# Kernel tuning notes

Hardware: AMD Instinct MI355X
Metric: run time of the kernel (lower is better)

The kernel has to match this reference:

```python
import jax, jax.numpy as jnp
import numpy as np
import math

NUM_HEADS = 8
KEY_SIZE = 512
EMBED_DIM = 256
BN_EPS = 1e-5


def batchnorm2d_train(x, w, b):
    # x: [B, H, N, hd]; channel axis = 1 (heads). Training-mode batch stats
    # over (B, N, hd), biased variance, as in torch BatchNorm2d forward.
    mean = jnp.mean(x, axis=(0, 2, 3), keepdims=True)
    var = jnp.mean((x - mean) ** 2, axis=(0, 2, 3), keepdims=True)
    xn = (x - mean) * jax.lax.rsqrt(var + BN_EPS)
    return xn * w[None, :, None, None] + b[None, :, None, None]


def l2_normalize(x, axis, eps=1e-12):
    # matches F.normalize(p=2): x / max(||x||, eps)
    n = jnp.sqrt(jnp.sum(x * x, axis=axis, keepdims=True))
    return x / jnp.maximum(n, eps)


def sparsemax(z, axis):
    # Euclidean projection onto the simplex along `axis` (Martins & Astudillo).
    K = z.shape[axis]
    z = z - jnp.max(z, axis=axis, keepdims=True)  # shift-invariant, for stability
    zs = jnp.flip(jnp.sort(z, axis=axis), axis=axis)  # descending sort
    rng_shape = [1] * z.ndim
    rng_shape[axis] = K
    rng = jnp.arange(1, K + 1, dtype=z.dtype).reshape(rng_shape)
    css = jnp.cumsum(zs, axis=axis)
    support = (1.0 + rng * zs) > css
    k_z = jnp.sum(support.astype(jnp.int32), axis=axis, keepdims=True)  # support size >= 1
    tau_sum = jnp.take_along_axis(css, k_z - 1, axis=axis)
    tau = (tau_sum - 1.0) / k_z.astype(z.dtype)
    return jnp.maximum(z - tau, 0.0)


def setup_inputs() -> dict:
    key = jax.random.key(0)
    k1, k2, k3 = jax.random.split(key, 3)
    B, N, C = 8, 1024, EMBED_DIM
    lim = 1.0 / math.sqrt(C)  # torch Linear default init range
    x = jax.random.normal(k1, (B, N, C), dtype=jnp.float32)
    qw = jax.random.uniform(k2, (KEY_SIZE, C), jnp.float32, -lim, lim)
    kw = jax.random.uniform(k3, (KEY_SIZE, C), jnp.float32, -lim, lim)
    bn_weight = jnp.ones((NUM_HEADS,), jnp.float32)
    bn_bias = jnp.zeros((NUM_HEADS,), jnp.float32)
    return {"x": x, "qw": qw, "kw": kw, "bn_weight": bn_weight, "bn_bias": bn_bias}


def reference(x, qw, kw, bn_weight, bn_bias):
    B, N, C = x.shape
    H = NUM_HEADS
    hd = KEY_SIZE // H
    q = jnp.einsum('bnc,kc->bnk', x, qw)  # [B,N,key_size]
    k = jnp.einsum('bnc,kc->bnk', x, kw)
    Q = q.reshape(B, N, H, hd).transpose(0, 2, 1, 3)  # [B,H,N,hd]
    K = k.reshape(B, N, H, hd).transpose(0, 2, 1, 3)
    Q = batchnorm2d_train(Q, bn_weight, bn_bias)
    K = batchnorm2d_train(K, bn_weight, bn_bias)
    Q = l2_normalize(Q, axis=3)
    K = l2_normalize(K, axis=3)
    scores = jnp.einsum('bhnd,bhmd->bhnm', Q, K) / math.sqrt(C)  # scale by sqrt(embeded_dim)
    scores = scores.transpose(0, 2, 1, 3).reshape(B, N, H * N)  # [B,N,H*N]
    # dropout is identity in eval mode
    return sparsemax(scores, axis=1)
```

## Files before the change

kernel.cpp:

```cpp
#include <hip/hip_runtime.h>
#include <math.h>

#define S_STAT 0
#define S_Q    32
#define S_K    (32 + 4194304)
#define S_PL   (32 + 8388608)
#define PLSZ   4194304

typedef unsigned short ushort;
typedef unsigned int uint;
typedef __attribute__((ext_vector_type(8))) short short8;
typedef __attribute__((ext_vector_type(16))) float floatx16;
typedef __attribute__((ext_vector_type(2))) float f32x2;

__device__ __forceinline__ float wave_sum(float v) {
#pragma unroll
    for (int m = 1; m < 64; m <<= 1) v += __shfl_xor(v, m);
    return v;
}

__device__ __forceinline__ ushort f2bf(float f) {
    uint u = __float_as_uint(f);
    uint r = (u + 0x7fffu + ((u >> 16) & 1u)) >> 16;
    return (ushort)r;
}

__global__ __launch_bounds__(64) void k0_zero(float* __restrict__ ws) {
    if (threadIdx.x < 32) ws[S_STAT + threadIdx.x] = 0.0f;
}

__global__ __launch_bounds__(256) void k_pre(const float* __restrict__ x,
                                             const float* __restrict__ qw,
                                             const float* __restrict__ kw,
                                             float* __restrict__ ws) {
    ushort* base = (ushort*)(ws + S_PL) + 4 * PLSZ;
    ushort* XH = base;
    ushort* XL = XH + 2097152;
    ushort* WH = XL + 2097152;
    ushort* WL = WH + 262144;
    const int bid = blockIdx.x;
    const int tid = threadIdx.x;
    const float* __restrict__ src;
    ushort *dh, *dl;
    int idx4;
    if (bid < 2048)      { src = x;  dh = XH;           dl = XL;           idx4 = bid * 256 + tid; }
    else if (bid < 2176) { src = qw; dh = WH;           dl = WL;           idx4 = (bid - 2048) * 256 + tid; }
    else                 { src = kw; dh = WH + 131072;  dl = WL + 131072;  idx4 = (bid - 2176) * 256 + tid; }
    const float4 v = *(const float4*)(src + (size_t)idx4 * 4);
    ushort4 hv, lv;
    {
        hv.x = f2bf(v.x); lv.x = f2bf(v.x - __uint_as_float(((uint)hv.x) << 16));
        hv.y = f2bf(v.y); lv.y = f2bf(v.y - __uint_as_float(((uint)hv.y) << 16));
        hv.z = f2bf(v.z); lv.z = f2bf(v.z - __uint_as_float(((uint)hv.z) << 16));
        hv.w = f2bf(v.w); lv.w = f2bf(v.w - __uint_as_float(((uint)hv.w) << 16));
    }
    *(ushort4*)(dh + (size_t)idx4 * 4) = hv;
    *(ushort4*)(dl + (size_t)idx4 * 4) = lv;
}

__global__ __launch_bounds__(256, 2) void k1_mfma(float* __restrict__ ws) {
    const ushort* base = (const ushort*)(ws + S_PL) + 4 * PLSZ;
    const ushort* __restrict__ XH = base;
    const ushort* __restrict__ XL = XH + 2097152;
    const ushort* __restrict__ WH = XL + 2097152;
    const ushort* __restrict__ WL = WH + 262144;
    const int t = threadIdx.x;
    const int l = t & 63;
    const int w = t >> 6;
    const int rw = w & 1, cw = w >> 1;
    const int row0 = blockIdx.x * 128 + rw * 64;
    const int col0 = blockIdx.y * 128 + cw * 64;
    const int lane31 = l & 31;
    const int kb8 = (l >> 5) * 8;

    floatx16 acc[2][2] = {};
#pragma unroll 4
    for (int kc = 0; kc < 256; kc += 16) {
        short8 ah[2], al[2], bh[2], bl[2];
#pragma unroll
        for (int rt = 0; rt < 2; ++rt) {
            const size_t o = (size_t)(row0 + rt * 32 + lane31) * 256 + kc + kb8;
            ah[rt] = *(const short8*)(XH + o);
            al[rt] = *(const short8*)(XL + o);
        }
#pragma unroll
        for (int ct = 0; ct < 2; ++ct) {
            const size_t o = (size_t)(col0 + ct * 32 + lane31) * 256 + kc + kb8;
            bh[ct] = *(const short8*)(WH + o);
            bl[ct] = *(const short8*)(WL + o);
        }
#pragma unroll
        for (int rt = 0; rt < 2; ++rt)
#pragma unroll
            for (int ct = 0; ct < 2; ++ct) {
                acc[rt][ct] = __builtin_amdgcn_mfma_f32_32x32x16_bf16(ah[rt], bh[ct], acc[rt][ct], 0, 0, 0);
                acc[rt][ct] = __builtin_amdgcn_mfma_f32_32x32x16_bf16(al[rt], bh[ct], acc[rt][ct], 0, 0, 0);
                acc[rt][ct] = __builtin_amdgcn_mfma_f32_32x32x16_bf16(ah[rt], bl[ct], acc[rt][ct], 0, 0, 0);
            }
    }

    const bool is_q = (col0 < 512);
    float* __restrict__ outp = ws + (is_q ? S_Q : S_K);
    const int cbase = col0 & 511;
    const int rsub = 4 * (l >> 5);
    float s1 = 0.f, s2 = 0.f;
#pragma unroll
    for (int rt = 0; rt < 2; ++rt)
#pragma unroll
        for (int ct = 0; ct < 2; ++ct)
#pragma unroll
            for (int e = 0; e < 16; ++e) {
                const int r = row0 + rt * 32 + rsub + (e & 3) + 8 * (e >> 2);
                const int c = cbase + ct * 32 + lane31;
                const float v = acc[rt][ct][e];
                outp[(size_t)r * 512 + c] = v;
                s1 += v; s2 += v * v;
            }
    s1 = wave_sum(s1);
    s2 = wave_sum(s2);
    if (l == 0) {
        const int head = (cbase >> 6) & 7;
        const int sb = (is_q ? 0 : 16) + head;
        atomicAdd(ws + S_STAT + sb, s1);
        atomicAdd(ws + S_STAT + sb + 8, s2);
    }
}

__global__ __launch_bounds__(256) void k3_norm(const float* __restrict__ bnw,
                                               const float* __restrict__ bnb,
                                               float* __restrict__ ws) {
    const int t = threadIdx.x;
    const int w = t >> 6, l = t & 63;
    const int nb = blockIdx.x;
    const int bh = blockIdx.y;
    const int b = bh >> 3, h = bh & 7;
    const int z = blockIdx.z;
    const float* __restrict__ in = ws + (z ? S_K : S_Q);
    const float* st = ws + S_STAT + (z ? 16 : 0);
    ushort* __restrict__ PH = (ushort*)(ws + S_PL) + (z ? 2 * PLSZ : 0) + (size_t)bh * 65536;
    ushort* __restrict__ PL = PH + PLSZ;
    const float inv_m = 1.0f / 524288.0f;
    const float mean  = st[h] * inv_m;
    const float var   = st[8 + h] * inv_m - mean * mean;
    const float alpha = rsqrtf(var + 1e-5f) * bnw[h];
    const float beta  = bnb[h] - mean * alpha;
    const float scale = z ? 0.0625f : 1.0f;

#pragma unroll 1
    for (int i = 0; i < 16; ++i) {
        const int n = nb * 64 + w * 16 + i;
        float v = in[(size_t)(b * 1024 + n) * 512 + h * 64 + l];
        v = fmaf(v, alpha, beta);
        float ss = wave_sum(v * v);
        v = v / fmaxf(sqrtf(ss), 1e-12f) * scale;
        ushort h16 = f2bf(v);
        float hif = __uint_as_float(((uint)h16) << 16);
        ushort l16 = f2bf(v - hif);
        const int idx = n * 64 + l;
        PH[idx] = h16;
        PL[idx] = l16;
    }
}

__global__ __launch_bounds__(256, 3) void k4_attn(const float* __restrict__ ws,
                                                  float* __restrict__ out) {
    __shared__ float part[4][4][32];
    const int t = threadIdx.x;
    const int l = t & 63;
    const int w = t >> 6;
    const int bid = blockIdx.x;
    const int bh = bid >> 5;
    const int j  = bid & 31;
    const int m0 = ((j & 7) << 7) + ((j >> 3) << 5);
    const int b = bh >> 3, h = bh & 7;
    const ushort* __restrict__ QH = (const ushort*)(ws + S_PL);
    const ushort* __restrict__ QL = QH + PLSZ;
    const ushort* __restrict__ KH = QH + 2 * PLSZ;
    const ushort* __restrict__ KL = QH + 3 * PLSZ;

    const int row = l & 31;
    const int kb8 = l >> 5;

    floatx16 acc[8] = {};

    const size_t koff = (size_t)(bh * 1024 + m0 + row) * 64 + kb8 * 8;
#pragma unroll
    for (int r = 0; r < 8; ++r) {
        const size_t qoff = (size_t)(bh * 1024 + w * 256 + r * 32 + row) * 64 + kb8 * 8;
#pragma unroll
        for (int ks = 0; ks < 4; ++ks) {
            short8 ah = *(const short8*)(QH + qoff + ks * 16);
            short8 al = *(const short8*)(QL + qoff + ks * 16);
            short8 kh = *(const short8*)(KH + koff + ks * 16);
            short8 kl = *(const short8*)(KL + koff + ks * 16);
            acc[r] = __builtin_amdgcn_mfma_f32_32x32x16_bf16(ah, kh, acc[r], 0, 0, 0);
            acc[r] = __builtin_amdgcn_mfma_f32_32x32x16_bf16(al, kh, acc[r], 0, 0, 0);
            acc[r] = __builtin_amdgcn_mfma_f32_32x32x16_bf16(ah, kl, acc[r], 0, 0, 0);
        }
    }

    const int col = row;

    {
        f32x2 sv = {0.f, 0.f};
#pragma unroll
        for (int r = 0; r < 8; ++r)
#pragma unroll
            for (int p = 0; p < 8; ++p) {
                f32x2 z2 = { acc[r][2 * p], acc[r][2 * p + 1] };
                sv += z2;
            }
        float vsuml = sv.x + sv.y;
        vsuml += __shfl_xor(vsuml, 32);
        if (l < 32) part[2][w][col] = vsuml;
    }
    __syncthreads();
    const float vsum = part[2][0][col] + part[2][1][col]
                     + part[2][2][col] + part[2][3][col];

    float tcur = (vsum - 1.0f) * (1.0f / 1024.0f);
    float tprev = tcur, sprev = 0.f;
#pragma unroll 1
    for (int it = 0; it < 6; ++it) {
        f32x2 s2v = {0.f, 0.f};
#pragma unroll
        for (int r = 0; r < 8; ++r) {
            f32x2 sr = {0.f, 0.f};
#pragma unroll
            for (int p = 0; p < 8; ++p) {
                f32x2 z2 = { acc[r][2 * p], acc[r][2 * p + 1] };
                f32x2 d = z2 - tcur;
                d.x = fmaxf(d.x, 0.f);
                d.y = fmaxf(d.y, 0.f);
                sr += d;
            }
            s2v += sr;
        }
        float sl = s2v.x + s2v.y;
        sl += __shfl_xor(sl, 32);
        if (l < 32) part[it & 1][w][col] = sl;
        __syncthreads();
        const float s = part[it & 1][0][col] + part[it & 1][1][col]
                      + part[it & 1][2][col] + part[it & 1][3][col];
        const float g = s - 1.0f;
        float step;
        if (it == 0) {
            step = g * (1.0f / 1024.0f);
        } else {
            const float denom = sprev - s;
            step = (denom > 1e-30f) ? g * (tcur - tprev) / denom : 0.f;
        }
        step = fmaxf(step, 0.f);
        tprev = tcur; sprev = s;
        tcur += step;
    }

    float cntl = 0.f, ssml = 0.f;
#pragma unroll
    for (int r = 0; r < 8; ++r)
#pragma unroll
        for (int e = 0; e < 16; ++e) {
            const float zz = acc[r][e];
            if (zz > tcur) { cntl += 1.f; ssml += zz; }
        }
    cntl += __shfl_xor(cntl, 32);
    ssml += __shfl_xor(ssml, 32);
    if (l < 32) { part[2][w][col] = cntl; part[3][w][col] = ssml; }
    __syncthreads();
    const float cnt  = part[2][0][col] + part[2][1][col] + part[2][2][col] + part[2][3][col];
    const float ssum = part[3][0][col] + part[3][1][col] + part[3][2][col] + part[3][3][col];
    const float tau = (ssum - 1.0f) / cnt;

    float* __restrict__ ob = out + (size_t)b * 1024 * 8192 + h * 1024 + m0 + col;
    const int nbase = w * 256 + 4 * kb8;
#pragma unroll
    for (int r = 0; r < 8; ++r)
#pragma unroll
        for (int e = 0; e < 16; ++e) {
            const int n = nbase + r * 32 + (e & 3) + 8 * (e >> 2);
            ob[(size_t)n * 8192] = fmaxf(acc[r][e] - tau, 0.f);
        }
}

extern "C" void kernel_launch(void* const* d_in, const int* in_sizes, int n_in,
                              void* d_out, int out_size, void* d_ws, size_t ws_size,
                              hipStream_t stream) {
    (void)in_sizes; (void)n_in; (void)out_size; (void)ws_size;
    const float* x   = (const float*)d_in[0];
    const float* qw  = (const float*)d_in[1];
    const float* kw  = (const float*)d_in[2];
    const float* bnw = (const float*)d_in[3];
    const float* bnb = (const float*)d_in[4];
    float* ws  = (float*)d_ws;
    float* out = (float*)d_out;

    hipLaunchKernelGGL(k0_zero, dim3(1), dim3(64), 0, stream, ws);
    hipLaunchKernelGGL(k_pre, dim3(2304), dim3(256), 0, stream, x, qw, kw, ws);
    hipLaunchKernelGGL(k1_mfma, dim3(64, 8), dim3(256), 0, stream, ws);
    hipLaunchKernelGGL(k3_norm, dim3(16, 64, 2), dim3(256), 0, stream, bnw, bnb, ws);
    hipLaunchKernelGGL(k4_attn, dim3(2048), dim3(256), 0, stream, ws, out);
}
```

Measured before the change: 442.8 us.

## Fold stats zeroing into k_pre, vectorize norm kernel, trim sparsemax iterations

Zeroing of the BN statistics buffer moves into the first block of k_pre, which removes a separate kernel launch. The norm kernel now has each thread load four floats and reduce over 16 lanes, so loads and stores are wider and the full-wave shuffle reductions are shorter. The iterative threshold search in the sparsemax stage runs five iterations instead of six. That cuts compute, but the threshold may converge less precisely and change outputs.

Result: no change. 440.1 us, median of 2 (-0.6%).

```diff
diff --git a/kernel.cpp b/kernel.cpp
--- a/kernel.cpp
+++ b/kernel.cpp
@@ -12,6 +12,7 @@
 typedef __attribute__((ext_vector_type(8))) short short8;
 typedef __attribute__((ext_vector_type(16))) float floatx16;
 typedef __attribute__((ext_vector_type(2))) float f32x2;
+typedef __attribute__((ext_vector_type(4))) float f32x4;
 
 __device__ __forceinline__ float wave_sum(float v) {
 #pragma unroll
@@ -23,10 +24,6 @@
     uint u = __float_as_uint(f);
     uint r = (u + 0x7fffu + ((u >> 16) & 1u)) >> 16;
     return (ushort)r;
-}
-
-__global__ __launch_bounds__(64) void k0_zero(float* __restrict__ ws) {
-    if (threadIdx.x < 32) ws[S_STAT + threadIdx.x] = 0.0f;
 }
 
 __global__ __launch_bounds__(256) void k_pre(const float* __restrict__ x,
@@ -40,6 +37,7 @@
     ushort* WL = WH + 262144;
     const int bid = blockIdx.x;
     const int tid = threadIdx.x;
+    if (bid == 0 && tid < 32) ws[S_STAT + tid] = 0.0f;
     const float* __restrict__ src;
     ushort *dh, *dl;
     int idx4;
@@ -131,6 +129,7 @@
                                                float* __restrict__ ws) {
     const int t = threadIdx.x;
     const int w = t >> 6, l = t & 63;
+    const int g = l >> 4, l16 = l & 15;
     const int nb = blockIdx.x;
     const int bh = blockIdx.y;
     const int b = bh >> 3, h = bh & 7;
@@ -146,19 +145,30 @@
     const float beta  = bnb[h] - mean * alpha;
     const float scale = z ? 0.0625f : 1.0f;
 
+    const int d0 = l16 * 4;
 #pragma unroll 1
-    for (int i = 0; i < 16; ++i) {
-        const int n = nb * 64 + w * 16 + i;
-        float v = in[(size_t)(b * 1024 + n) * 512 + h * 64 + l];
-        v = fmaf(v, alpha, beta);
-        float ss = wave_sum(v * v);
-        v = v / fmaxf(sqrtf(ss), 1e-12f) * scale;
-        ushort h16 = f2bf(v);
-        float hif = __uint_as_float(((uint)h16) << 16);
-        ushort l16 = f2bf(v - hif);
-        const int idx = n * 64 + l;
-        PH[idx] = h16;
-        PL[idx] = l16;
+    for (int i = 0; i < 4; ++i) {
+        const int n = nb * 64 + w * 16 + i * 4 + g;
+        const f32x4 vv = *(const f32x4*)&in[(size_t)(b * 1024 + n) * 512 + h * 64 + d0];
+        float v0 = fmaf(vv.x, alpha, beta);
+        float v1 = fmaf(vv.y, alpha, beta);
+        float v2 = fmaf(vv.z, alpha, beta);
+        float v3 = fmaf(vv.w, alpha, beta);
+        float ss = v0 * v0 + v1 * v1 + v2 * v2 + v3 * v3;
+        ss += __shfl_xor(ss, 1);
+        ss += __shfl_xor(ss, 2);
+        ss += __shfl_xor(ss, 4);
+        ss += __shfl_xor(ss, 8);
+        const float inv = scale / fmaxf(sqrtf(ss), 1e-12f);
+        v0 *= inv; v1 *= inv; v2 *= inv; v3 *= inv;
+        ushort4 hv, lv;
+        hv.x = f2bf(v0); lv.x = f2bf(v0 - __uint_as_float(((uint)hv.x) << 16));
+        hv.y = f2bf(v1); lv.y = f2bf(v1 - __uint_as_float(((uint)hv.y) << 16));
+        hv.z = f2bf(v2); lv.z = f2bf(v2 - __uint_as_float(((uint)hv.z) << 16));
+        hv.w = f2bf(v3); lv.w = f2bf(v3 - __uint_as_float(((uint)hv.w) << 16));
+        const int idx = n * 64 + d0;
+        *(ushort4*)&PH[idx] = hv;
+        *(ushort4*)&PL[idx] = lv;
     }
 }
 
@@ -221,7 +231,7 @@
     float tcur = (vsum - 1.0f) * (1.0f / 1024.0f);
     float tprev = tcur, sprev = 0.f;
 #pragma unroll 1
-    for (int it = 0; it < 6; ++it) {
+    for (int it = 0; it < 5; ++it) {
         f32x2 s2v = {0.f, 0.f};
 #pragma unroll
         for (int r = 0; r < 8; ++r) {
@@ -294,7 +304,6 @@
     float* ws  = (float*)d_ws;
     float* out = (float*)d_out;
 
-    hipLaunchKernelGGL(k0_zero, dim3(1), dim3(64), 0, stream, ws);
     hipLaunchKernelGGL(k_pre, dim3(2304), dim3(256), 0, stream, x, qw, kw, ws);
     hipLaunchKernelGGL(k1_mfma, dim3(64, 8), dim3(256), 0, stream, ws);
     hipLaunchKernelGGL(k3_norm, dim3(16, 64, 2), dim3(256), 0, stream, bnw, bnb, ws);
```
